# Kernel tuning notes

Measured on AMD Instinct MI355X. Metric: run time of the kernel, lower is better.

The kernel has to match this reference:

```python
import jax, jax.numpy as jnp
import numpy as np
import math

B, H, W = 2, 64, 64
D_MODEL = 192
D_STATE = 16
EXPAND = 1
D_INNER = EXPAND * D_MODEL
DT_RANK = math.ceil(D_MODEL / 16)  # 'auto' -> 12
DT_MIN, DT_MAX, DT_FLOOR = 0.001, 0.1, 0.0001


def setup_inputs() -> dict:
    key = jax.random.key(0)
    ks = jax.random.split(key, 10)
    x = jax.random.normal(ks[0], (B, H, W, D_MODEL), jnp.float32)
    in_proj_w = jax.random.normal(ks[1], (D_INNER, D_MODEL), jnp.float32) * (D_MODEL ** -0.5)
    in_proj_b = jnp.zeros((D_INNER,), jnp.float32)
    x_proj_w = jax.random.normal(ks[2], (2 * DT_RANK + 3 * D_STATE, D_INNER), jnp.float32) * (D_INNER ** -0.5)
    dt_init_std = DT_RANK ** -0.5
    dt_projT_w = jax.random.uniform(ks[3], (D_INNER, DT_RANK), jnp.float32, -dt_init_std, dt_init_std)
    dt_projL_w = jax.random.uniform(ks[4], (D_INNER, DT_RANK), jnp.float32, -dt_init_std, dt_init_std)
    # dt bias init: inverse-softplus of dt sampled log-uniform in [dt_min, dt_max]
    dt = jnp.exp(jax.random.uniform(ks[5], (D_INNER,), jnp.float32) * (math.log(DT_MAX) - math.log(DT_MIN)) + math.log(DT_MIN))
    dt = jnp.clip(dt, DT_FLOOR, None)
    inv_dt = dt + jnp.log(-jnp.expm1(-dt))
    dt_projT_b = inv_dt
    dt_projL_b = inv_dt
    A_init = jnp.tile(jnp.arange(1, D_STATE + 1, dtype=jnp.float32), (D_INNER, 1))  # [D_INNER, N]
    AT_log = jnp.log(A_init)
    AL_log = jnp.log(A_init)
    D_skip = jnp.ones((D_INNER,), jnp.float32)
    out_proj_w = jax.random.normal(ks[6], (D_MODEL, D_INNER), jnp.float32) * (D_INNER ** -0.5)
    out_proj_b = jnp.zeros((D_MODEL,), jnp.float32)
    return {"x": x, "in_proj_w": in_proj_w, "in_proj_b": in_proj_b, "x_proj_w": x_proj_w,
            "dt_projT_w": dt_projT_w, "dt_projT_b": dt_projT_b, "dt_projL_w": dt_projL_w,
            "dt_projL_b": dt_projL_b, "AT_log": AT_log, "AL_log": AL_log, "D_skip": D_skip,
            "out_proj_w": out_proj_w, "out_proj_b": out_proj_b}


def _wavefront_ssm(u, x_proj_w, dt_projT_w, dt_projT_b, dt_projL_w, dt_projL_b, AT_log, AL_log, D_skip):
    # u: [B,H,W,D_INNER]. 2D selective scan: state at (i,j) mixes top (i-1,j) and left (i,j-1).
    R, N = DT_RANK, D_STATE
    proj = jnp.einsum('bhwd,pd->bhwp', u, x_proj_w)  # [B,H,W,2R+3N]
    dtT_r = proj[..., :R]
    dtL_r = proj[..., R:2 * R]
    B_T = proj[..., 2 * R:2 * R + N]            # [B,H,W,N]
    B_L = proj[..., 2 * R + N:2 * R + 2 * N]    # [B,H,W,N]
    C = proj[..., 2 * R + 2 * N:]               # [B,H,W,N]
    deltaT = jax.nn.softplus(jnp.einsum('bhwr,dr->bhwd', dtT_r, dt_projT_w) + dt_projT_b)  # [B,H,W,D]
    deltaL = jax.nn.softplus(jnp.einsum('bhwr,dr->bhwd', dtL_r, dt_projL_w) + dt_projL_b)
    AT = -jnp.exp(AT_log)  # [D,N]
    AL = -jnp.exp(AL_log)
    dAT = jnp.exp(deltaT[..., None] * AT)  # [B,H,W,D,N]
    dAL = jnp.exp(deltaL[..., None] * AL)
    dB = (deltaT[..., None] * B_T[..., None, :] + deltaL[..., None] * B_L[..., None, :]) * u[..., None]  # [B,H,W,D,N]
    # reorder to [H,W,B,D,N] for scanning
    dAT_s = jnp.transpose(dAT, (1, 2, 0, 3, 4))
    dAL_s = jnp.transpose(dAL, (1, 2, 0, 3, 4))
    dB_s = jnp.transpose(dB, (1, 2, 0, 3, 4))

    def row_step(h_prev_row, row):  # h_prev_row: [W,B,D,N]
        dAT_r, dAL_r, dB_r = row
        top = dAT_r * h_prev_row + dB_r  # top-neighbor contribution + input, per column

        def col_step(h_left, cols):  # h_left: [B,D,N]
            t, a = cols
            h = t + a * h_left
            return h, h

        h0 = jnp.zeros_like(h_prev_row[0])
        _, h_row = jax.lax.scan(col_step, h0, (top, dAL_r))  # [W,B,D,N]
        return h_row, h_row

    h_init = jnp.zeros((W, u.shape[0], D_INNER, N), u.dtype)
    _, hs = jax.lax.scan(row_step, h_init, (dAT_s, dAL_s, dB_s))  # [H,W,B,D,N]
    h = jnp.transpose(hs, (2, 0, 1, 3, 4))  # [B,H,W,D,N]
    y = jnp.einsum('bhwdn,bhwn->bhwd', h, C) + u * D_skip
    return y


def reference(x, in_proj_w, in_proj_b, x_proj_w, dt_projT_w, dt_projT_b,
              dt_projL_w, dt_projL_b, AT_log, AL_log, D_skip, out_proj_w, out_proj_b):
    u = jax.nn.gelu(jnp.einsum('bhwc,dc->bhwd', x, in_proj_w) + in_proj_b, approximate=False)
    y = _wavefront_ssm(u, x_proj_w, dt_projT_w, dt_projT_b, dt_projL_w, dt_projL_b, AT_log, AL_log, D_skip)
    y = jax.nn.gelu(y, approximate=False)
    out = jnp.einsum('bhwd,cd->bhwc', y, out_proj_w) + out_proj_b
    return out
```

## Files before the change

kernel.cpp:

```cpp
#include <hip/hip_runtime.h>
#include <math.h>

#define DM 192
#define RNK 12
#define NS 16
#define NO2 432

#define OFF_FLAG   156672u
#define OFF_PY0    156688u
#define OFF_PY1    1729552u
#define OFF_YG     3302416u
#define OFF_DIAG   5268496u
#define OFF_TL2    6841360u
#define OFF_BC4D   9987088u

typedef __attribute__((ext_vector_type(8))) short short8v;
typedef __attribute__((ext_vector_type(4))) float floatx4;

__device__ __forceinline__ float gelu_f(float x){
    return 0.5f * x * (1.0f + erff(x * 0.70710678118654752f));
}
__device__ __forceinline__ float softplus_f(float x){
    return fmaxf(x, 0.0f) + log1pf(__expf(-fabsf(x)));
}
__device__ __forceinline__ int diag_off(int s){
    return (s <= 64) ? ((s * (s + 1)) >> 1) : (2080 + (((s - 64) * (191 - s)) >> 1));
}
__device__ __forceinline__ void inv_diag(int q, int& i_out, int& j_out){
    int s;
    if (q < 2080){
        s = (int)((sqrtf(8.0f * (float)q + 1.0f) - 1.0f) * 0.5f);
        while (((s + 1) * (s + 2)) / 2 <= q) s++;
        while ((s * (s + 1)) / 2 > q) s--;
    } else {
        const int q2 = 4095 - q;
        int t = (int)((sqrtf(8.0f * (float)q2 + 1.0f) - 1.0f) * 0.5f);
        while (((t + 1) * (t + 2)) / 2 <= q2) t++;
        while ((t * (t + 1)) / 2 > q2) t--;
        s = 126 - t;
    }
    const int jmin = (s > 63) ? (s - 63) : 0;
    const int j = jmin + (q - diag_off(s));
    j_out = j;
    i_out = s - j;
}
__device__ __forceinline__ unsigned short bf16_rte(float f){
    unsigned u = __float_as_uint(f);
    unsigned r = (u + 0x7fffu + ((u >> 16) & 1u)) >> 16;
    return (unsigned short)r;
}
__device__ __forceinline__ float bf16_f(unsigned short h){
    return __uint_as_float(((unsigned)h) << 16);
}
__device__ __forceinline__ void split8(float4 v0, float4 v1, short8v& hi, short8v& lo){
    float f[8] = {v0.x, v0.y, v0.z, v0.w, v1.x, v1.y, v1.z, v1.w};
    #pragma unroll
    for (int e = 0; e < 8; e++){
        unsigned short h = bf16_rte(f[e]);
        hi[e] = (short)h;
        lo[e] = (short)bf16_rte(f[e] - bf16_f(h));
    }
}

#define SW_WINH 0u
#define SW_WINL 36864u
#define SW_WCH  73728u
#define SW_WCL  156672u
#define SW_WOH  239616u
#define SW_WOL  276480u

__global__ __launch_bounds__(256) void prep_k(const float* __restrict__ Win,
                                              const float* __restrict__ xpw,
                                              const float* __restrict__ dtwT,
                                              const float* __restrict__ dtwL,
                                              const float* __restrict__ Wout,
                                              const float* __restrict__ ATl,
                                              const float* __restrict__ ALl,
                                              float* __restrict__ ws){
    unsigned short* __restrict__ wsu = (unsigned short*)ws;
    if (blockIdx.x == 612){
        __shared__ int okf;
        if (threadIdx.x == 0) okf = 1;
        __syncthreads();
        bool ok = true;
        for (int t = threadIdx.x; t < 6144; t += 256){
            const float* arr = (t < 3072) ? ATl : ALl;
            int e = (t < 3072) ? t : t - 3072;
            int n = e & 15;
            ok = ok && (fabsf(arr[e] - logf((float)(n + 1))) < 1e-5f);
        }
        if (!ok) atomicAnd(&okf, 0);
        __syncthreads();
        if (threadIdx.x == 0) ws[OFF_FLAG] = okf ? 1.0f : 0.0f;
        return;
    }
    int idx = blockIdx.x * 256 + threadIdx.x;
    float w;
    unsigned hioff, looff, rel;
    if (idx < 36864){
        w = Win[idx]; hioff = SW_WINH; looff = SW_WINL; rel = idx;
    } else if (idx < 119808){
        int t = idx - 36864;
        int o = t / DM, c = t - o * DM;
        float acc = 0.f;
        if (o < 192){
            #pragma unroll
            for (int r = 0; r < RNK; r++) acc += dtwT[o * RNK + r] * xpw[r * DM + c];
        } else if (o < 384){
            int d2 = o - 192;
            #pragma unroll
            for (int r = 0; r < RNK; r++) acc += dtwL[d2 * RNK + r] * xpw[(RNK + r) * DM + c];
        } else {
            acc = xpw[(2 * RNK + (o - 384)) * DM + c];
        }
        w = acc; hioff = SW_WCH; looff = SW_WCL; rel = t;
    } else if (idx < 156672){
        int t = idx - 119808;
        w = Wout[t]; hioff = SW_WOH; looff = SW_WOL; rel = t;
    } else return;
    unsigned short h = bf16_rte(w);
    wsu[hioff + rel] = h;
    wsu[looff + rel] = bf16_rte(w - bf16_f(h));
}

__global__ __launch_bounds__(256) void proj_k(const float* __restrict__ x,
                                              const float* __restrict__ inb,
                                              const float* __restrict__ dtTb,
                                              const float* __restrict__ dtLb,
                                              float* __restrict__ ws){
    __shared__ float u_t[16][196];
    __shared__ float g2[16][436];
    const unsigned short* __restrict__ wsu = (const unsigned short*)ws;
    const int bx = blockIdx.x;
    const int b = bx >> 8;
    const int Q0 = (bx & 255) * 16;
    const int tid = threadIdx.x;
    const int wv = tid >> 6, lane = tid & 63;
    const int lr = lane & 15, lg = lane >> 4;

    int ic, jc;
    inv_diag(Q0 + lr, ic, jc);
    const size_t xrow = ((size_t)(b << 12) + (size_t)(ic * 64 + jc)) * 192;

    short8v xh[6], xl[6];
    #pragma unroll
    for (int ks = 0; ks < 6; ks++){
        const float* xp = x + xrow + ks * 32 + lg * 8;
        split8(*(const float4*)xp, *(const float4*)(xp + 4), xh[ks], xl[ks]);
    }
    {
        floatx4 ac0 = {0.f,0.f,0.f,0.f}, ac1 = {0.f,0.f,0.f,0.f}, ac2 = {0.f,0.f,0.f,0.f};
        const int n0 = wv * 48;
        #pragma unroll
        for (int ks = 0; ks < 6; ks++){
            const size_t rb = (size_t)(n0 + lr) * 192 + ks * 32 + lg * 8;
            const short8v bh0 = *(const short8v*)(wsu + SW_WINH + rb);
            const short8v bl0 = *(const short8v*)(wsu + SW_WINL + rb);
            const short8v bh1 = *(const short8v*)(wsu + SW_WINH + rb + 16*192);
            const short8v bl1 = *(const short8v*)(wsu + SW_WINL + rb + 16*192);
            const short8v bh2 = *(const short8v*)(wsu + SW_WINH + rb + 32*192);
            const short8v bl2 = *(const short8v*)(wsu + SW_WINL + rb + 32*192);
            ac0 = __builtin_amdgcn_mfma_f32_16x16x32_bf16(xh[ks], bh0, ac0, 0, 0, 0);
            ac1 = __builtin_amdgcn_mfma_f32_16x16x32_bf16(xh[ks], bh1, ac1, 0, 0, 0);
            ac2 = __builtin_amdgcn_mfma_f32_16x16x32_bf16(xh[ks], bh2, ac2, 0, 0, 0);
            ac0 = __builtin_amdgcn_mfma_f32_16x16x32_bf16(xh[ks], bl0, ac0, 0, 0, 0);
            ac1 = __builtin_amdgcn_mfma_f32_16x16x32_bf16(xh[ks], bl1, ac1, 0, 0, 0);
            ac2 = __builtin_amdgcn_mfma_f32_16x16x32_bf16(xh[ks], bl2, ac2, 0, 0, 0);
            ac0 = __builtin_amdgcn_mfma_f32_16x16x32_bf16(xl[ks], bh0, ac0, 0, 0, 0);
            ac1 = __builtin_amdgcn_mfma_f32_16x16x32_bf16(xl[ks], bh1, ac1, 0, 0, 0);
            ac2 = __builtin_amdgcn_mfma_f32_16x16x32_bf16(xl[ks], bh2, ac2, 0, 0, 0);
        }
        const float b0 = inb[n0 + lr], b1 = inb[n0 + 16 + lr], b2 = inb[n0 + 32 + lr];
        #pragma unroll
        for (int r = 0; r < 4; r++){
            const int pl = lg * 4 + r;
            u_t[pl][n0 + lr]      = gelu_f(ac0[r] + b0);
            u_t[pl][n0 + 16 + lr] = gelu_f(ac1[r] + b1);
            u_t[pl][n0 + 32 + lr] = gelu_f(ac2[r] + b2);
        }
    }
    __syncthreads();

    {
        float* __restrict__ u_dg = ws + OFF_DIAG;
        #pragma unroll
        for (int pass = 0; pass < 3; pass++){
            const int plane = pass * 64 + (tid >> 2);
            const int posq = (tid & 3) * 4;
            float4 v = make_float4(u_t[posq + 0][plane], u_t[posq + 1][plane],
                                   u_t[posq + 2][plane], u_t[posq + 3][plane]);
            *(float4*)&u_dg[(size_t)(b * 192 + plane) * 4096 + Q0 + posq] = v;
        }
    }

    short8v uh[6], ul[6];
    #pragma unroll
    for (int ks = 0; ks < 6; ks++){
        const float* up = &u_t[lr][ks * 32 + lg * 8];
        split8(*(const float4*)up, *(const float4*)(up + 4), uh[ks], ul[ks]);
    }
    const int t0 = wv * 7;
    const int cnt = (wv == 3) ? 6 : 7;
    for (int tp = 0; tp < cnt; tp += 2){
        const bool dual = (tp + 1 < cnt);
        const int n0a = (t0 + tp) * 16, n0b = dual ? (t0 + tp + 1) * 16 : n0a;
        floatx4 acA = {0.f,0.f,0.f,0.f}, acB = {0.f,0.f,0.f,0.f};
        #pragma unroll
        for (int ks = 0; ks < 6; ks++){
            const size_t ra = (size_t)(n0a + lr) * 192 + ks * 32 + lg * 8;
            const short8v bhA = *(const short8v*)(wsu + SW_WCH + ra);
            const short8v blA = *(const short8v*)(wsu + SW_WCL + ra);
            acA = __builtin_amdgcn_mfma_f32_16x16x32_bf16(uh[ks], bhA, acA, 0, 0, 0);
            acA = __builtin_amdgcn_mfma_f32_16x16x32_bf16(uh[ks], blA, acA, 0, 0, 0);
            acA = __builtin_amdgcn_mfma_f32_16x16x32_bf16(ul[ks], bhA, acA, 0, 0, 0);
            if (dual){
                const size_t rbb = (size_t)(n0b + lr) * 192 + ks * 32 + lg * 8;
                const short8v bhB = *(const short8v*)(wsu + SW_WCH + rbb);
                const short8v blB = *(const short8v*)(wsu + SW_WCL + rbb);
                acB = __builtin_amdgcn_mfma_f32_16x16x32_bf16(uh[ks], bhB, acB, 0, 0, 0);
                acB = __builtin_amdgcn_mfma_f32_16x16x32_bf16(uh[ks], blB, acB, 0, 0, 0);
                acB = __builtin_amdgcn_mfma_f32_16x16x32_bf16(ul[ks], bhB, acB, 0, 0, 0);
            }
        }
        #pragma unroll
        for (int half = 0; half < 2; half++){
            if (half == 1 && !dual) break;
            const floatx4 ac = half ? acB : acA;
            const int o = (half ? n0b : n0a) + lr;
            float bb = 0.f; int mode = 2;
            if (o < 192){ bb = dtTb[o]; mode = 0; }
            else if (o < 384){ bb = dtLb[o - 192]; mode = 1; }
            #pragma unroll
            for (int r = 0; r < 4; r++){
                float v = ac[r];
                if (mode < 2) v = softplus_f(v + bb);
                g2[lg * 4 + r][o] = v;
            }
        }
    }
    __syncthreads();

    {
        float* __restrict__ tl_dg = ws + OFF_TL2;
        const int plane = tid >> 2;
        const int posq = (tid & 3) * 4;
        #pragma unroll
        for (int pass = 0; pass < 3; pass++){
            const int o = pass * 64 + plane;
            float4 w0 = make_float4(g2[posq + 0][o], g2[posq + 0][192 + o],
                                    g2[posq + 1][o], g2[posq + 1][192 + o]);
            float4 w1 = make_float4(g2[posq + 2][o], g2[posq + 2][192 + o],
                                    g2[posq + 3][o], g2[posq + 3][192 + o]);
            float* base = &tl_dg[(size_t)(b * 192 + o) * 8192 + (size_t)(Q0 + posq) * 2];
            *(float4*)&base[0] = w0;
            *(float4*)&base[4] = w1;
        }
        if (tid < 192){
            const int pl = tid >> 4;
            const int pos = tid & 15;
            float4 v = *(float4*)&g2[pos][384 + pl * 4];
            float4* dst = (float4*)(ws + OFF_BC4D) + (size_t)(b * 12 + pl) * 4096 + Q0 + pos;
            *dst = v;
        }
    }
}

#define LOADSET(pfx, sv) do {                                                   \
    const int sc_ = (sv) < 126 ? (sv) : 126;                                    \
    const int jmin_ = (sc_ > 63) ? (sc_ - 63) : 0;                              \
    pfx##_q = diag_off(sc_) - jmin_ + j;                                        \
    pfx##_u = pu[pfx##_q];                                                      \
    pfx##_tv = ptl[pfx##_q];                                                    \
    pfx##_bt = pBT[pfx##_q]; pfx##_bl = pBL[pfx##_q]; pfx##_cc = pC[pfx##_q];   \
} while (0)

#define STEP(pfx, sv) do {                                                      \
    const float dT_ = pfx##_tv.x, dL_ = pfx##_tv.y, u_ = pfx##_u;               \
    const float bt_[4] = {pfx##_bt.x, pfx##_bt.y, pfx##_bt.z, pfx##_bt.w};      \
    const float bl_[4] = {pfx##_bl.x, pfx##_bl.y, pfx##_bl.z, pfx##_bl.w};      \
    const float cc_[4] = {pfx##_cc.x, pfx##_cc.y, pfx##_cc.z, pfx##_cc.w};      \
    const int q_ = pfx##_q;                                                     \
    LOADSET(pfx, (sv) + 4);                                                     \
    float da_[4], dl_[4];                                                       \
    if (sflag){                                                                 \
        const float E_ = __expf(-dT_), F_ = __expf(-dL_);                       \
        da_[0] = __expf(nA1 * dT_); dl_[0] = __expf(nA1 * dL_);                 \
        da_[1] = da_[0] * E_; da_[2] = da_[1] * E_; da_[3] = da_[2] * E_;       \
        dl_[1] = dl_[0] * F_; dl_[2] = dl_[1] * F_; dl_[3] = dl_[2] * F_;       \
    } else {                                                                    \
        da_[0] = __expf(dT_ * ATr[0]); da_[1] = __expf(dT_ * ATr[1]);           \
        da_[2] = __expf(dT_ * ATr[2]); da_[3] = __expf(dT_ * ATr[3]);           \
        dl_[0] = __expf(dL_ * ALr[0]); dl_[1] = __expf(dL_ * ALr[1]);           \
        dl_[2] = __expf(dL_ * ALr[2]); dl_[3] = __expf(dL_ * ALr[3]);           \
    }                                                                           \
    const int ic_ = (sv) - j;                                                   \
    const bool act_ = ((unsigned)ic_) < 64u;                                    \
    const float udT_ = u_ * dT_, udL_ = u_ * dL_;                               \
    float y_ = 0.f;                                                             \
    _Pragma("unroll")                                                           \
    for (int k = 0; k < 4; k++){                                                \
        float hl_ = __shfl_up(h[k], 1u, 64);                                    \
        hl_ = (j == 0) ? 0.f : hl_;                                             \
        float hn_ = fmaf(da_[k], h[k], fmaf(dl_[k], hl_, fmaf(udT_, bt_[k], udL_ * bl_[k]))); \
        h[k] = act_ ? hn_ : h[k];                                               \
        y_ = fmaf(hn_, cc_[k], y_);                                             \
    }                                                                           \
    if (act_) ylds[(wv << 12) + q_] = y_;                                       \
} while (0)

__global__ __launch_bounds__(256) void scan_k(const float* __restrict__ ATl,
                                              const float* __restrict__ ALl,
                                              const float* __restrict__ Dskp,
                                              float* __restrict__ ws){
    __shared__ float ylds[4 * 4096];
    const int bd = blockIdx.x;
    const int b = bd / 192, d = bd - b * 192;
    const int tid = threadIdx.x;
    const int wv = tid >> 6, j = tid & 63;
    const int n0 = wv * 4;
    const int ng = wv;

    const float* __restrict__ pu = ws + OFF_DIAG + (size_t)bd * 4096;
    const float2* __restrict__ ptl = (const float2*)(ws + OFF_TL2 + (size_t)bd * 8192);
    const float4* __restrict__ bc4 = (const float4*)(ws + OFF_BC4D) + (size_t)(b * 12) * 4096;
    const float4* __restrict__ pBT = bc4 + (size_t)(0 + ng) * 4096;
    const float4* __restrict__ pBL = bc4 + (size_t)(4 + ng) * 4096;
    const float4* __restrict__ pC  = bc4 + (size_t)(8 + ng) * 4096;

    const bool sflag = (ws[OFF_FLAG] > 0.5f);
    const float nA1 = -(float)(n0 + 1);
    float ATr[4], ALr[4];
    if (!sflag){
        #pragma unroll
        for (int k = 0; k < 4; k++){
            ATr[k] = -expf(ATl[d * NS + n0 + k]);
            ALr[k] = -expf(ALl[d * NS + n0 + k]);
        }
    } else {
        #pragma unroll
        for (int k = 0; k < 4; k++){ ATr[k] = 0.f; ALr[k] = 0.f; }
    }
    float h[4] = {0.f, 0.f, 0.f, 0.f};

    int a_q, b_q, c_q, d_q;
    float a_u; float2 a_tv; float4 a_bt, a_bl, a_cc;
    float b_u; float2 b_tv; float4 b_bt, b_bl, b_cc;
    float c_u; float2 c_tv; float4 c_bt, c_bl, c_cc;
    float d_u; float2 d_tv; float4 d_bt, d_bl, d_cc;
    LOADSET(a, 0);
    LOADSET(b, 1);
    LOADSET(c, 2);
    LOADSET(d, 3);

    for (int s = 0; s < 128; s += 4){
        STEP(a, s);
        STEP(b, s + 1);
        STEP(c, s + 2);
        STEP(d, s + 3);
    }

    __syncthreads();
    const float Dsk = Dskp[d];
    for (int idx = tid; idx < 4096; idx += 256){
        const float v = ylds[idx] + ylds[4096 + idx] + ylds[8192 + idx] + ylds[12288 + idx]
                      + pu[idx] * Dsk;
        ylds[idx] = gelu_f(v);
    }
    __syncthreads();
    float* __restrict__ yg = ws + OFF_YG + (size_t)bd * 4096;
    for (int idx = tid; idx < 4096; idx += 256){
        const int i = idx >> 6, jj = idx & 63;
        const int s = i + jj;
        const int jmin = (s > 63) ? (s - 63) : 0;
        yg[idx] = ylds[diag_off(s) + jj - jmin];
    }
}

__global__ __launch_bounds__(256) void out_k(const float* __restrict__ Wob,
                                             float* __restrict__ ws,
                                             float* __restrict__ out){
    __shared__ float yg_t[16][196];
    const unsigned short* __restrict__ wsu = (const unsigned short*)ws;
    const int P0 = blockIdx.x * 16;
    const int b = P0 >> 12;
    const int prel = P0 & 4095;
    const int tid = threadIdx.x;

    {
        const float* __restrict__ ygp = ws + OFF_YG;
        #pragma unroll
        for (int pass = 0; pass < 3; pass++){
            const int plane = pass * 64 + (tid >> 2);
            const int posq = (tid & 3) * 4;
            float4 v = *(const float4*)&ygp[(size_t)(b * 192 + plane) * 4096 + prel + posq];
            yg_t[posq + 0][plane] = v.x;
            yg_t[posq + 1][plane] = v.y;
            yg_t[posq + 2][plane] = v.z;
            yg_t[posq + 3][plane] = v.w;
        }
    }
    __syncthreads();

    const int wv = tid >> 6, lane = tid & 63;
    const int lr = lane & 15, lg = lane >> 4;

    short8v yh[6], yl2[6];
    #pragma unroll
    for (int ks = 0; ks < 6; ks++){
        const float* yp = &yg_t[lr][ks * 32 + lg * 8];
        split8(*(const float4*)yp, *(const float4*)(yp + 4), yh[ks], yl2[ks]);
    }
    {
        floatx4 ac0 = {0.f,0.f,0.f,0.f}, ac1 = {0.f,0.f,0.f,0.f}, ac2 = {0.f,0.f,0.f,0.f};
        const int n0 = wv * 48;
        #pragma unroll
        for (int ks = 0; ks < 6; ks++){
            const size_t rb = (size_t)(n0 + lr) * 192 + ks * 32 + lg * 8;
            const short8v bh0 = *(const short8v*)(wsu + SW_WOH + rb);
            const short8v bl0 = *(const short8v*)(wsu + SW_WOL + rb);
            const short8v bh1 = *(const short8v*)(wsu + SW_WOH + rb + 16*192);
            const short8v bl1 = *(const short8v*)(wsu + SW_WOL + rb + 16*192);
            const short8v bh2 = *(const short8v*)(wsu + SW_WOH + rb + 32*192);
            const short8v bl2 = *(const short8v*)(wsu + SW_WOL + rb + 32*192);
            ac0 = __builtin_amdgcn_mfma_f32_16x16x32_bf16(yh[ks], bh0, ac0, 0, 0, 0);
            ac1 = __builtin_amdgcn_mfma_f32_16x16x32_bf16(yh[ks], bh1, ac1, 0, 0, 0);
            ac2 = __builtin_amdgcn_mfma_f32_16x16x32_bf16(yh[ks], bh2, ac2, 0, 0, 0);
            ac0 = __builtin_amdgcn_mfma_f32_16x16x32_bf16(yh[ks], bl0, ac0, 0, 0, 0);
            ac1 = __builtin_amdgcn_mfma_f32_16x16x32_bf16(yh[ks], bl1, ac1, 0, 0, 0);
            ac2 = __builtin_amdgcn_mfma_f32_16x16x32_bf16(yh[ks], bl2, ac2, 0, 0, 0);
            ac0 = __builtin_amdgcn_mfma_f32_16x16x32_bf16(yl2[ks], bh0, ac0, 0, 0, 0);
            ac1 = __builtin_amdgcn_mfma_f32_16x16x32_bf16(yl2[ks], bh1, ac1, 0, 0, 0);
            ac2 = __builtin_amdgcn_mfma_f32_16x16x32_bf16(yl2[ks], bh2, ac2, 0, 0, 0);
        }
        const float b0 = Wob[n0 + lr], b1 = Wob[n0 + 16 + lr], b2 = Wob[n0 + 32 + lr];
        #pragma unroll
        for (int r = 0; r < 4; r++){
            const int pos = P0 + lg * 4 + r;
            out[(size_t)pos * 192 + n0 + lr]      = ac0[r] + b0;
            out[(size_t)pos * 192 + n0 + 16 + lr] = ac1[r] + b1;
            out[(size_t)pos * 192 + n0 + 32 + lr] = ac2[r] + b2;
        }
    }
}

extern "C" void kernel_launch(void* const* d_in, const int* in_sizes, int n_in,
                              void* d_out, int out_size, void* d_ws, size_t ws_size,
                              hipStream_t stream) {
    const float* x    = (const float*)d_in[0];
    const float* Win  = (const float*)d_in[1];
    const float* Winb = (const float*)d_in[2];
    const float* xpw  = (const float*)d_in[3];
    const float* dtTw = (const float*)d_in[4];
    const float* dtTb = (const float*)d_in[5];
    const float* dtLw = (const float*)d_in[6];
    const float* dtLb = (const float*)d_in[7];
    const float* ATl  = (const float*)d_in[8];
    const float* ALl  = (const float*)d_in[9];
    const float* Dsk  = (const float*)d_in[10];
    const float* Wo   = (const float*)d_in[11];
    const float* Wob  = (const float*)d_in[12];
    float* out = (float*)d_out;
    float* ws  = (float*)d_ws;

    hipLaunchKernelGGL(prep_k,   dim3(613), dim3(256), 0, stream, Win, xpw, dtTw, dtLw, Wo, ATl, ALl, ws);
    hipLaunchKernelGGL(proj_k,   dim3(512), dim3(256), 0, stream, x, Winb, dtTb, dtLb, ws);
    hipLaunchKernelGGL(scan_k,   dim3(384), dim3(256), 0, stream, ATl, ALl, Dsk, ws);
    hipLaunchKernelGGL(out_k,    dim3(512), dim3(256), 0, stream, Wob, ws, out);
}
```

Before: 113.5 us.

## Stage u and dt diagonals through double-buffered LDS; store partial y in bf16

The scan kernel now reads the per-channel u and dT/dL diagonal data in 16-diagonal chunks. Each chunk is loaded cooperatively from global memory into double-buffered shared memory, and the loads for the next chunk are issued while the current chunk is processed. Previously each lane read these values per step directly from global memory. The per-wave partial y values in LDS are also stored as bf16 rather than fp32, halving the ylds footprint so the new buffers fit and occupancy can rise. In exchange there is a block barrier per chunk and some precision loss in the partial sums and the gelu output before they are written back.

```diff
diff --git a/kernel.cpp b/kernel.cpp
--- a/kernel.cpp
+++ b/kernel.cpp
@@ -269,17 +269,18 @@
     const int sc_ = (sv) < 126 ? (sv) : 126;                                    \
     const int jmin_ = (sc_ > 63) ? (sc_ - 63) : 0;                              \
     pfx##_q = diag_off(sc_) - jmin_ + j;                                        \
-    pfx##_u = pu[pfx##_q];                                                      \
-    pfx##_tv = ptl[pfx##_q];                                                    \
     pfx##_bt = pBT[pfx##_q]; pfx##_bl = pBL[pfx##_q]; pfx##_cc = pC[pfx##_q];   \
 } while (0)
 
 #define STEP(pfx, sv) do {                                                      \
-    const float dT_ = pfx##_tv.x, dL_ = pfx##_tv.y, u_ = pfx##_u;               \
+    const int q_ = pfx##_q;                                                     \
+    int r_ = q_ - base; r_ = (r_ < 0) ? 0 : r_;                                 \
+    const float u_ = ubuf[buf][r_];                                             \
+    const float2 tv_ = *(const float2*)&tlbuf[buf][2 * r_];                     \
+    const float dT_ = tv_.x, dL_ = tv_.y;                                       \
     const float bt_[4] = {pfx##_bt.x, pfx##_bt.y, pfx##_bt.z, pfx##_bt.w};      \
     const float bl_[4] = {pfx##_bl.x, pfx##_bl.y, pfx##_bl.z, pfx##_bl.w};      \
     const float cc_[4] = {pfx##_cc.x, pfx##_cc.y, pfx##_cc.z, pfx##_cc.w};      \
-    const int q_ = pfx##_q;                                                     \
     LOADSET(pfx, (sv) + 4);                                                     \
     float da_[4], dl_[4];                                                       \
     if (sflag){                                                                 \
@@ -305,14 +306,16 @@
         h[k] = act_ ? hn_ : h[k];                                               \
         y_ = fmaf(hn_, cc_[k], y_);                                             \
     }                                                                           \
-    if (act_) ylds[(wv << 12) + q_] = y_;                                       \
+    if (act_) ylds[(wv << 12) + q_] = bf16_rte(y_);                             \
 } while (0)
 
 __global__ __launch_bounds__(256) void scan_k(const float* __restrict__ ATl,
                                               const float* __restrict__ ALl,
                                               const float* __restrict__ Dskp,
                                               float* __restrict__ ws){
-    __shared__ float ylds[4 * 4096];
+    __shared__ unsigned short ylds[4 * 4096];
+    __shared__ float ubuf[2][1024];
+    __shared__ float tlbuf[2][2048];
     const int bd = blockIdx.x;
     const int b = bd / 192, d = bd - b * 192;
     const int tid = threadIdx.x;
@@ -321,7 +324,7 @@
     const int ng = wv;
 
     const float* __restrict__ pu = ws + OFF_DIAG + (size_t)bd * 4096;
-    const float2* __restrict__ ptl = (const float2*)(ws + OFF_TL2 + (size_t)bd * 8192);
+    const float* __restrict__ ptl0 = ws + OFF_TL2 + (size_t)bd * 8192;
     const float4* __restrict__ bc4 = (const float4*)(ws + OFF_BC4D) + (size_t)(b * 12) * 4096;
     const float4* __restrict__ pBT = bc4 + (size_t)(0 + ng) * 4096;
     const float4* __restrict__ pBL = bc4 + (size_t)(4 + ng) * 4096;
@@ -342,29 +345,61 @@
     }
     float h[4] = {0.f, 0.f, 0.f, 0.f};
 
+    {
+        const float4* gu = (const float4*)pu;
+        const float4* gt = (const float4*)ptl0;
+        if (tid < 34) *(float4*)&ubuf[0][tid << 2] = gu[tid];
+        if (tid < 68) *(float4*)&tlbuf[0][tid << 2] = gt[tid];
+    }
+    __syncthreads();
+
     int a_q, b_q, c_q, d_q;
-    float a_u; float2 a_tv; float4 a_bt, a_bl, a_cc;
-    float b_u; float2 b_tv; float4 b_bt, b_bl, b_cc;
-    float c_u; float2 c_tv; float4 c_bt, c_bl, c_cc;
-    float d_u; float2 d_tv; float4 d_bt, d_bl, d_cc;
+    float4 a_bt, a_bl, a_cc;
+    float4 b_bt, b_bl, b_cc;
+    float4 c_bt, c_bl, c_cc;
+    float4 d_bt, d_bl, d_cc;
     LOADSET(a, 0);
     LOADSET(b, 1);
     LOADSET(c, 2);
     LOADSET(d, 3);
 
-    for (int s = 0; s < 128; s += 4){
-        STEP(a, s);
-        STEP(b, s + 1);
-        STEP(c, s + 2);
-        STEP(d, s + 3);
-    }
-
-    __syncthreads();
+    int base = 0;
+    for (int ch = 0; ch < 8; ch++){
+        const int buf = ch & 1;
+        float4 su = {0,0,0,0}, st0 = {0,0,0,0}, st1 = {0,0,0,0};
+        int un4 = 0, tn4 = 0;
+        if (ch < 7){
+            const int nb = diag_off(16 * (ch + 1));
+            const int ne = diag_off(16 * (ch + 2));
+            un4 = (ne - nb) >> 2;
+            tn4 = un4 << 1;
+            const float4* gu = (const float4*)(pu + nb);
+            const float4* gt = (const float4*)(ptl0 + 2 * nb);
+            if (tid < un4) su = gu[tid];
+            if (tid < tn4) st0 = gt[tid];
+            if (tid + 256 < tn4) st1 = gt[tid + 256];
+        }
+        const int s0 = ch << 4;
+        STEP(a, s0 + 0);  STEP(b, s0 + 1);  STEP(c, s0 + 2);  STEP(d, s0 + 3);
+        STEP(a, s0 + 4);  STEP(b, s0 + 5);  STEP(c, s0 + 6);  STEP(d, s0 + 7);
+        STEP(a, s0 + 8);  STEP(b, s0 + 9);  STEP(c, s0 + 10); STEP(d, s0 + 11);
+        STEP(a, s0 + 12); STEP(b, s0 + 13); STEP(c, s0 + 14); STEP(d, s0 + 15);
+        if (ch < 7){
+            const int nbuf = buf ^ 1;
+            if (tid < un4) *(float4*)&ubuf[nbuf][tid << 2] = su;
+            if (tid < tn4) *(float4*)&tlbuf[nbuf][tid << 2] = st0;
+            if (tid + 256 < tn4) *(float4*)&tlbuf[nbuf][(tid + 256) << 2] = st1;
+            base = diag_off(16 * (ch + 1));
+        }
+        __syncthreads();
+    }
+
     const float Dsk = Dskp[d];
     for (int idx = tid; idx < 4096; idx += 256){
-        const float v = ylds[idx] + ylds[4096 + idx] + ylds[8192 + idx] + ylds[12288 + idx]
-                      + pu[idx] * Dsk;
-        ylds[idx] = gelu_f(v);
+        const float v = bf16_f(ylds[idx]) + bf16_f(ylds[4096 + idx]) +
+                        bf16_f(ylds[8192 + idx]) + bf16_f(ylds[12288 + idx]) +
+                        pu[idx] * Dsk;
+        ylds[idx] = bf16_rte(gelu_f(v));
     }
     __syncthreads();
     float* __restrict__ yg = ws + OFF_YG + (size_t)bd * 4096;
@@ -372,7 +407,7 @@
         const int i = idx >> 6, jj = idx & 63;
         const int s = i + jj;
         const int jmin = (s > 63) ? (s - 63) : 0;
-        yg[idx] = ylds[diag_off(s) + jj - jmin];
+        yg[idx] = bf16_f(ylds[diag_off(s) + jj - jmin]);
     }
 }
 
```

Result: no change. 114.8 us (+1.1%).

## Stream scan inputs through an LDS ring via global_load_lds and store partials in bf16

Applied to the files above, without the earlier changes.

The wavefront scan kernel no longer prefetches each diagonal's u, dt, B and C values into registers four steps ahead. Instead it issues asynchronous global-to-LDS loads into a three-slot per-wave ring and waits with an explicit vmcnt so two diagonals stay in flight. This is meant to cut register pressure and hide global latency. The per-wave y partial sums and the gelu output are now held in LDS as bf16 rather than fp32. That halves the storage for that buffer but adds rounding error to the output and raises total LDS use because of the ring.

```diff
diff --git a/kernel.cpp b/kernel.cpp
--- a/kernel.cpp
+++ b/kernel.cpp
@@ -16,6 +16,13 @@
 
 typedef __attribute__((ext_vector_type(8))) short short8v;
 typedef __attribute__((ext_vector_type(4))) float floatx4;
+
+#define GLDS4(g, l)  __builtin_amdgcn_global_load_lds( \
+    (const __attribute__((address_space(1))) void*)(g), \
+    (__attribute__((address_space(3))) void*)(l), 4, 0, 0)
+#define GLDS16(g, l) __builtin_amdgcn_global_load_lds( \
+    (const __attribute__((address_space(1))) void*)(g), \
+    (__attribute__((address_space(3))) void*)(l), 16, 0, 0)
 
 __device__ __forceinline__ float gelu_f(float x){
     return 0.5f * x * (1.0f + erff(x * 0.70710678118654752f));
@@ -265,54 +272,12 @@
     }
 }
 
-#define LOADSET(pfx, sv) do {                                                   \
-    const int sc_ = (sv) < 126 ? (sv) : 126;                                    \
-    const int jmin_ = (sc_ > 63) ? (sc_ - 63) : 0;                              \
-    pfx##_q = diag_off(sc_) - jmin_ + j;                                        \
-    pfx##_u = pu[pfx##_q];                                                      \
-    pfx##_tv = ptl[pfx##_q];                                                    \
-    pfx##_bt = pBT[pfx##_q]; pfx##_bl = pBL[pfx##_q]; pfx##_cc = pC[pfx##_q];   \
-} while (0)
-
-#define STEP(pfx, sv) do {                                                      \
-    const float dT_ = pfx##_tv.x, dL_ = pfx##_tv.y, u_ = pfx##_u;               \
-    const float bt_[4] = {pfx##_bt.x, pfx##_bt.y, pfx##_bt.z, pfx##_bt.w};      \
-    const float bl_[4] = {pfx##_bl.x, pfx##_bl.y, pfx##_bl.z, pfx##_bl.w};      \
-    const float cc_[4] = {pfx##_cc.x, pfx##_cc.y, pfx##_cc.z, pfx##_cc.w};      \
-    const int q_ = pfx##_q;                                                     \
-    LOADSET(pfx, (sv) + 4);                                                     \
-    float da_[4], dl_[4];                                                       \
-    if (sflag){                                                                 \
-        const float E_ = __expf(-dT_), F_ = __expf(-dL_);                       \
-        da_[0] = __expf(nA1 * dT_); dl_[0] = __expf(nA1 * dL_);                 \
-        da_[1] = da_[0] * E_; da_[2] = da_[1] * E_; da_[3] = da_[2] * E_;       \
-        dl_[1] = dl_[0] * F_; dl_[2] = dl_[1] * F_; dl_[3] = dl_[2] * F_;       \
-    } else {                                                                    \
-        da_[0] = __expf(dT_ * ATr[0]); da_[1] = __expf(dT_ * ATr[1]);           \
-        da_[2] = __expf(dT_ * ATr[2]); da_[3] = __expf(dT_ * ATr[3]);           \
-        dl_[0] = __expf(dL_ * ALr[0]); dl_[1] = __expf(dL_ * ALr[1]);           \
-        dl_[2] = __expf(dL_ * ALr[2]); dl_[3] = __expf(dL_ * ALr[3]);           \
-    }                                                                           \
-    const int ic_ = (sv) - j;                                                   \
-    const bool act_ = ((unsigned)ic_) < 64u;                                    \
-    const float udT_ = u_ * dT_, udL_ = u_ * dL_;                               \
-    float y_ = 0.f;                                                             \
-    _Pragma("unroll")                                                           \
-    for (int k = 0; k < 4; k++){                                                \
-        float hl_ = __shfl_up(h[k], 1u, 64);                                    \
-        hl_ = (j == 0) ? 0.f : hl_;                                             \
-        float hn_ = fmaf(da_[k], h[k], fmaf(dl_[k], hl_, fmaf(udT_, bt_[k], udL_ * bl_[k]))); \
-        h[k] = act_ ? hn_ : h[k];                                               \
-        y_ = fmaf(hn_, cc_[k], y_);                                             \
-    }                                                                           \
-    if (act_) ylds[(wv << 12) + q_] = y_;                                       \
-} while (0)
-
 __global__ __launch_bounds__(256) void scan_k(const float* __restrict__ ATl,
                                               const float* __restrict__ ALl,
                                               const float* __restrict__ Dskp,
                                               float* __restrict__ ws){
-    __shared__ float ylds[4 * 4096];
+    __shared__ float ring[3][4][960];
+    __shared__ unsigned short ylds[4 * 4096];
     const int bd = blockIdx.x;
     const int b = bd / 192, d = bd - b * 192;
     const int tid = threadIdx.x;
@@ -321,7 +286,7 @@
     const int ng = wv;
 
     const float* __restrict__ pu = ws + OFF_DIAG + (size_t)bd * 4096;
-    const float2* __restrict__ ptl = (const float2*)(ws + OFF_TL2 + (size_t)bd * 8192);
+    const float* __restrict__ ptlf = ws + OFF_TL2 + (size_t)bd * 8192;
     const float4* __restrict__ bc4 = (const float4*)(ws + OFF_BC4D) + (size_t)(b * 12) * 4096;
     const float4* __restrict__ pBT = bc4 + (size_t)(0 + ng) * 4096;
     const float4* __restrict__ pBL = bc4 + (size_t)(4 + ng) * 4096;
@@ -342,29 +307,76 @@
     }
     float h[4] = {0.f, 0.f, 0.f, 0.f};
 
-    int a_q, b_q, c_q, d_q;
-    float a_u; float2 a_tv; float4 a_bt, a_bl, a_cc;
-    float b_u; float2 b_tv; float4 b_bt, b_bl, b_cc;
-    float c_u; float2 c_tv; float4 c_bt, c_bl, c_cc;
-    float d_u; float2 d_tv; float4 d_bt, d_bl, d_cc;
-    LOADSET(a, 0);
-    LOADSET(b, 1);
-    LOADSET(c, 2);
-    LOADSET(d, 3);
-
-    for (int s = 0; s < 128; s += 4){
-        STEP(a, s);
-        STEP(b, s + 1);
-        STEP(c, s + 2);
-        STEP(d, s + 3);
+    #define ISSUE(sl, sv) do {                                                  \
+        const int sc2_ = (sv) < 126 ? (sv) : 126;                               \
+        const int jmin2_ = (sc2_ > 63) ? (sc2_ - 63) : 0;                       \
+        const int q2_ = diag_off(sc2_) - jmin2_ + j;                            \
+        float* lb_ = &ring[sl][wv][0];                                          \
+        GLDS4(pu + q2_, lb_);                                                   \
+        GLDS4(ptlf + 2 * q2_,     lb_ + 64);                                    \
+        GLDS4(ptlf + 2 * q2_ + 1, lb_ + 128);                                   \
+        GLDS16(pBT + q2_, lb_ + 192);                                           \
+        GLDS16(pBL + q2_, lb_ + 448);                                           \
+        GLDS16(pC  + q2_, lb_ + 704);                                           \
+    } while (0)
+
+    ISSUE(0, 0);
+    ISSUE(1, 1);
+
+    for (int s = 0; s < 127; s++){
+        const int sl2 = (s + 2) % 3;
+        ISSUE(sl2, s + 2);
+        __builtin_amdgcn_sched_barrier(0);
+        asm volatile("s_waitcnt vmcnt(12)" ::: "memory");
+        __builtin_amdgcn_sched_barrier(0);
+
+        const float* lb = &ring[s % 3][wv][0];
+        const float u_  = lb[j];
+        const float dT_ = lb[64 + j];
+        const float dL_ = lb[128 + j];
+        const float4 bt4 = *(const float4*)&lb[192 + 4 * j];
+        const float4 bl4 = *(const float4*)&lb[448 + 4 * j];
+        const float4 cc4 = *(const float4*)&lb[704 + 4 * j];
+        const float bt_[4] = {bt4.x, bt4.y, bt4.z, bt4.w};
+        const float bl_[4] = {bl4.x, bl4.y, bl4.z, bl4.w};
+        const float cc_[4] = {cc4.x, cc4.y, cc4.z, cc4.w};
+
+        float da_[4], dl_[4];
+        if (sflag){
+            const float E_ = __expf(-dT_), F_ = __expf(-dL_);
+            da_[0] = __expf(nA1 * dT_); dl_[0] = __expf(nA1 * dL_);
+            da_[1] = da_[0] * E_; da_[2] = da_[1] * E_; da_[3] = da_[2] * E_;
+            dl_[1] = dl_[0] * F_; dl_[2] = dl_[1] * F_; dl_[3] = dl_[2] * F_;
+        } else {
+            da_[0] = __expf(dT_ * ATr[0]); da_[1] = __expf(dT_ * ATr[1]);
+            da_[2] = __expf(dT_ * ATr[2]); da_[3] = __expf(dT_ * ATr[3]);
+            dl_[0] = __expf(dL_ * ALr[0]); dl_[1] = __expf(dL_ * ALr[1]);
+            dl_[2] = __expf(dL_ * ALr[2]); dl_[3] = __expf(dL_ * ALr[3]);
+        }
+        const int ic_ = s - j;
+        const bool act_ = ((unsigned)ic_) < 64u;
+        const int jmin_ = (s > 63) ? (s - 63) : 0;
+        const int q_ = diag_off(s) - jmin_ + j;
+        const float udT_ = u_ * dT_, udL_ = u_ * dL_;
+        float y_ = 0.f;
+        #pragma unroll
+        for (int k = 0; k < 4; k++){
+            float hl_ = __shfl_up(h[k], 1u, 64);
+            hl_ = (j == 0) ? 0.f : hl_;
+            float hn_ = fmaf(da_[k], h[k], fmaf(dl_[k], hl_, fmaf(udT_, bt_[k], udL_ * bl_[k])));
+            h[k] = act_ ? hn_ : h[k];
+            y_ = fmaf(hn_, cc_[k], y_);
+        }
+        if (act_) ylds[(wv << 12) + q_] = bf16_rte(y_);
     }
 
     __syncthreads();
     const float Dsk = Dskp[d];
     for (int idx = tid; idx < 4096; idx += 256){
-        const float v = ylds[idx] + ylds[4096 + idx] + ylds[8192 + idx] + ylds[12288 + idx]
-                      + pu[idx] * Dsk;
-        ylds[idx] = gelu_f(v);
+        const float v = bf16_f(ylds[idx]) + bf16_f(ylds[4096 + idx]) +
+                        bf16_f(ylds[8192 + idx]) + bf16_f(ylds[12288 + idx]) +
+                        pu[idx] * Dsk;
+        ylds[idx] = bf16_rte(gelu_f(v));
     }
     __syncthreads();
     float* __restrict__ yg = ws + OFF_YG + (size_t)bd * 4096;
@@ -372,7 +384,7 @@
         const int i = idx >> 6, jj = idx & 63;
         const int s = i + jj;
         const int jmin = (s > 63) ? (s - 63) : 0;
-        yg[idx] = ylds[diag_off(s) + jj - jmin];
+        yg[idx] = bf16_f(ylds[diag_off(s) + jj - jmin]);
     }
 }
 
```

New measurement: 167.7 us. 1.48x slower.
